# Kernel tuning notes

Hardware: AMD Instinct MI355X
Metric: run time of the kernel (lower is better)

The kernel has to match this reference:

```python
import jax, jax.numpy as jnp
import numpy as np

LAYERS, BLOCKS = 10, 4
RC, DC, SC, EC = 32, 32, 256, 256  # residual, dilation, skip, end channels
CIN, COUT, K = 6, 1, 2
DILATIONS = [2 ** (i % LAYERS) for i in range(BLOCKS * LAYERS)]
NL = len(DILATIONS)


def conv1d(x, w, dilation=1, pad=0):
    # x: [N, C, T], w: [O, I, K]
    return jax.lax.conv_general_dilated(
        x, w, window_strides=(1,), padding=[(pad, pad)],
        rhs_dilation=(dilation,), dimension_numbers=('NCH', 'OIH', 'NCH'))


def setup_inputs() -> dict:
    key = jax.random.key(0)
    ks = jax.random.split(key, 10)
    s = 0.1
    return {
        'x': jax.random.normal(ks[0], (8, CIN, 8192), dtype=jnp.float32),
        'start_w': jax.random.normal(ks[1], (RC, CIN, 1), dtype=jnp.float32) * s,
        'filter_w': jax.random.normal(ks[2], (NL, DC, RC, K), dtype=jnp.float32) * s,
        'gate_w': jax.random.normal(ks[3], (NL, DC, RC, K), dtype=jnp.float32) * s,
        'res_w': jax.random.normal(ks[4], (NL, RC, DC, 1), dtype=jnp.float32) * s,
        'skip_w': jax.random.normal(ks[5], (NL, SC, DC, 1), dtype=jnp.float32) * s,
        'end1_w': jax.random.normal(ks[6], (EC, SC, 1), dtype=jnp.float32) * s,
        'end1_b': jax.random.normal(ks[7], (EC,), dtype=jnp.float32) * s,
        'end2_w': jax.random.normal(ks[8], (COUT, EC, 1), dtype=jnp.float32) * s,
        'end2_b': jax.random.normal(ks[9], (COUT,), dtype=jnp.float32) * s,
    }


def reference(x, start_w, filter_w, gate_w, res_w, skip_w, end1_w, end1_b, end2_w, end2_b):
    x = conv1d(x, start_w)  # [B, RC, T]
    T = x.shape[2]
    # symmetric padding=(K-1)*d makes length grow by d each layer;
    # the shortest skip is the first one: T + (K-1)*DILATIONS[0]
    min_len = T + (K - 1) * DILATIONS[0]
    skip_sum = jnp.zeros((x.shape[0], SC, min_len), dtype=x.dtype)
    for i, d in enumerate(DILATIONS):
        pad = (K - 1) * d
        f = jnp.tanh(conv1d(x, filter_w[i], d, pad))
        g = jax.nn.sigmoid(conv1d(x, gate_w[i], d, pad))
        x = f * g  # [B, DC, T'] with T' = T_prev + d
        s = conv1d(x, skip_w[i])
        skip_sum = skip_sum + s[:, :, -min_len:]
        x = conv1d(x, res_w[i]) + x  # residual add (RC == DC)
    h = jax.nn.relu(skip_sum)
    h = jax.nn.relu(conv1d(h, end1_w) + end1_b[None, :, None])
    h = conv1d(h, end2_w) + end2_b[None, :, None]
    return h[:, :, -1]  # [B, COUT]
```

## Files before the change

kernel.cpp:

```cpp
#include <hip/hip_runtime.h>
#include <hip/hip_fp16.h>
#include <math.h>


#define NL 40
#define TLEN 8192

#define F_BLOB 0
#define F_C0   40960
#define F_Z    41216
#define F_H    51456
#define F_OB   53504
#define F_CNT  53512
#define F_DUMP 60000

typedef __attribute__((ext_vector_type(2))) _Float16 h2;

#if defined(__has_builtin)
#if __has_builtin(__builtin_amdgcn_fdot2)
#define HAS_FDOT2 1
#endif
#endif

__device__ __forceinline__ float FDOT2(h2 a, h2 b, float c) {
#ifdef HAS_FDOT2
    return __builtin_amdgcn_fdot2(a, b, c, false);
#else
    return c + (float)a.x * (float)b.x + (float)a.y * (float)b.y;
#endif
}

__device__ __forceinline__ float tanh_fast(float f) {
    f = fminf(fmaxf(f, -15.f), 15.f);
    float e2 = __expf(2.f * f);
    return (e2 - 1.f) / (e2 + 1.f);
}

__global__ __launch_bounds__(256) void k1_fold(
    const float* __restrict__ x, const float* __restrict__ start_w,
    const float* __restrict__ filter_w, const float* __restrict__ gate_w,
    const float* __restrict__ res_w, float* __restrict__ ws)
{
    const int l = blockIdx.x, m = blockIdx.y;
    const int t = threadIdx.x;

    if (l == NL) {
        if (m == 0) {
            const int b = t >> 5, ch = t & 31;
            float acc = 0.f;
#pragma unroll
            for (int j = 0; j < 6; ++j)
                acc += start_w[ch * 6 + j] * x[(b * 6 + j) * TLEN + TLEN - 1];
            ws[F_C0 + t] = acc;
            if (t < 8) { ws[F_OB + t] = 0.f; ((int*)(ws + F_CNT))[t] = 0; }
        } else {
            for (int k = t; k < 2048; k += 256) ws[F_H + k] = 0.f;
        }
        return;
    }

    __shared__ float F[32][32];
    __shared__ __align__(16) float R[32][36];
    const float* src = m ? gate_w : filter_w;
    for (int e = t; e < 1024; e += 256)
        F[e >> 5][e & 31] = src[(l * 1024 + e) * 2];
    if (l > 0)
        for (int e = t; e < 1024; e += 256) {
            const int k = e >> 5, j = e & 31;
            R[k][j] = res_w[(l - 1) * 1024 + e] + (k == j ? 1.f : 0.f);
        }
    __syncthreads();

    const int ch = t >> 3, jg = t & 7, j0 = jg * 4;
    float o0, o1, o2, o3;
    if (l == 0) {
        o0 = F[ch][j0]; o1 = F[ch][j0+1]; o2 = F[ch][j0+2]; o3 = F[ch][j0+3];
    } else {
        o0 = o1 = o2 = o3 = 0.f;
#pragma unroll
        for (int k = 0; k < 32; ++k) {
            const float fv = F[ch][k];
            const float4 rv = *(const float4*)&R[k][j0];
            o0 += fv * rv.x; o1 += fv * rv.y; o2 += fv * rv.z; o3 += fv * rv.w;
        }
    }
    const int hh = jg >> 2;
    __half* dst = (__half*)ws + (size_t)l * 2048 + (hh * 32 + ch) * 32
                + (m ? 16 : 0) + (j0 & 15);
    ((__half2*)dst)[0] = __floats2half2_rn(o0, o1);
    ((__half2*)dst)[1] = __floats2half2_rn(o2, o3);
}

#define K2_PREF(L, W) do {                                                   \
    if ((L) < NL) {                                                          \
        _Pragma("unroll")                                                    \
        for (int i = 0; i < 4; ++i)                                          \
            W[i] = blob[(L) * 256 + lane * 4 + i];                           \
    }                                                                        \
} while (0)

#define K2_STEP(L, W) do {                                                   \
         \
    float zx = __shfl_xor(z, 1, 64);                                         \
    float ze = (ch & 1) ? zx : z;                                            \
    float zo = (ch & 1) ? z  : zx;                                           \
    __half2 pk = __halves2half2(__float2half(ze), __float2half(zo));         \
    int pki; __builtin_memcpy(&pki, &pk, 4);                                 \
    h2 sv[8];                                                                \
    _Pragma("unroll")                                                        \
    for (int i = 0; i < 8; ++i) {                                            \
        int q = __shfl(pki, hbase + 2 * i, 64);                              \
        __builtin_memcpy(&sv[i], &q, 4);                                     \
    }                                                                        \
    float f = 0.f, g = 0.f;                                                  \
    const h2* wf = (const h2*)&W[0];                                         \
    const h2* wg = (const h2*)&W[2];                                         \
    _Pragma("unroll")                                                        \
    for (int i = 0; i < 8; ++i) {                                            \
        f = FDOT2(wf[i], sv[i], f);                                          \
        g = FDOT2(wg[i], sv[i], g);                                          \
    }                                                                        \
    f += __shfl_xor(f, 32, 64);                                              \
    g += __shfl_xor(g, 32, 64);                                              \
    z = tanh_fast(f) * (1.f / (1.f + __expf(-g)));                           \
    if (h == 0) zbuf[((L) * 8 + b) * 32 + ch] = z;                           \
    K2_PREF((L) + 4, W);                                                     \
} while (0)

__global__ __launch_bounds__(256) void k2_recur(
    const float* __restrict__ skip_w, const float* __restrict__ end1_w,
    const float* __restrict__ end1_b, const float* __restrict__ end2_w,
    float* __restrict__ ws)
{
    const int bi = blockIdx.x, t = threadIdx.x;

    if (bi >= 8) {
        const int wi = (bi - 8) * 256 + t;
        const float4* s4 = (const float4*)skip_w;
        const float4* e4 = (const float4*)end1_w;
        float acc = 0.f;
        for (int i = wi; i < 81920; i += 32768) acc += s4[i].x;
        if (wi < 16384) acc += e4[wi].x;
        if (wi < 64) acc += end2_w[wi * 4] + end1_b[wi * 4];
        if (acc == 1234.567f) ws[F_DUMP] = acc;
        return;
    }
    if (t >= 64) return;

    const int b = bi, lane = t;
    const int ch = lane & 31, h = lane >> 5, hbase = h << 4;
    float* zbuf = ws + F_Z;
    float z = ws[F_C0 + b * 32 + ch];

    const float4* blob = (const float4*)ws;
    float4 w0[4], w1[4], w2[4], w3[4];
    K2_PREF(0, w0); K2_PREF(1, w1); K2_PREF(2, w2); K2_PREF(3, w3);
    for (int l = 0; l < NL; l += 4) {
        K2_STEP(l + 0, w0);
        K2_STEP(l + 1, w1);
        K2_STEP(l + 2, w2);
        K2_STEP(l + 3, w3);
    }
}

__global__ __launch_bounds__(256) void k3a_skip(
    const float* __restrict__ skip_w, float* __restrict__ ws)
{
    const int l = blockIdx.x, b = blockIdx.y, t = threadIdx.x;
    __shared__ __align__(16) float zsm[32];
    if (t < 32) zsm[t] = ws[F_Z + (l * 8 + b) * 32 + t];
    __syncthreads();
    const float4* w4 = (const float4*)(skip_w + (size_t)(l * 256 + t) * 32);
    const float4* z4 = (const float4*)zsm;
    float acc = 0.f;
#pragma unroll
    for (int i = 0; i < 8; ++i) {
        float4 wv = w4[i], zv = z4[i];
        acc += wv.x*zv.x + wv.y*zv.y + wv.z*zv.z + wv.w*zv.w;
    }
    atomicAdd(&ws[F_H + b * 256 + t], acc);
}

__global__ __launch_bounds__(256) void k3b_end(
    const float* __restrict__ end1_w, const float* __restrict__ end1_b,
    const float* __restrict__ end2_w, const float* __restrict__ end2_b,
    float* __restrict__ ws, float* __restrict__ out)
{
    const int q = blockIdx.x, b = blockIdx.y, t = threadIdx.x;
    __shared__ __align__(16) float hsm[256];
    __shared__ float psum[64][5];
    const int p = t >> 6, oc = t & 63, row = q * 64 + oc;

    float4 wreg[16];
    const float4* wp = (const float4*)(end1_w + (size_t)row * 256 + p * 64);
#pragma unroll
    for (int i = 0; i < 16; ++i) wreg[i] = wp[i];

    hsm[t] = fmaxf(ws[F_H + b * 256 + t], 0.f);
    __syncthreads();
    const float4* h4 = (const float4*)(hsm + p * 64);
    float acc = 0.f;
#pragma unroll
    for (int i = 0; i < 16; ++i) {
        float4 wv = wreg[i], hv = h4[i];
        acc += wv.x*hv.x + wv.y*hv.y + wv.z*hv.z + wv.w*hv.w;
    }
    psum[oc][p] = acc;
    __syncthreads();
    if (t < 64) {
        const int rr = q * 64 + t;
        float e = psum[t][0] + psum[t][1] + psum[t][2] + psum[t][3]
                + end1_b[rr];
        e = fmaxf(e, 0.f);
        float pe = e * end2_w[rr];
#pragma unroll
        for (int off = 32; off > 0; off >>= 1)
            pe += __shfl_down(pe, off, 64);
        if (t == 0) {
            float* obuf = ws + F_OB;
            int* cnt = (int*)(ws + F_CNT);
            atomicAdd(&obuf[b], pe);
            __threadfence();
            int old = __hip_atomic_fetch_add(&cnt[b], 1, __ATOMIC_ACQ_REL,
                                             __HIP_MEMORY_SCOPE_AGENT);
            if (old == 3) {
                float tot = __hip_atomic_load(&obuf[b], __ATOMIC_ACQUIRE,
                                              __HIP_MEMORY_SCOPE_AGENT);
                out[b] = tot + end2_b[0];
            }
        }
    }
}

extern "C" void kernel_launch(void* const* d_in, const int* in_sizes, int n_in,
                              void* d_out, int out_size, void* d_ws, size_t ws_size,
                              hipStream_t stream) {
    const float* x        = (const float*)d_in[0];
    const float* start_w  = (const float*)d_in[1];
    const float* filter_w = (const float*)d_in[2];
    const float* gate_w   = (const float*)d_in[3];
    const float* res_w    = (const float*)d_in[4];
    const float* skip_w   = (const float*)d_in[5];
    const float* end1_w   = (const float*)d_in[6];
    const float* end1_b   = (const float*)d_in[7];
    const float* end2_w   = (const float*)d_in[8];
    const float* end2_b   = (const float*)d_in[9];
    float* out = (float*)d_out;
    float* ws  = (float*)d_ws;

    k1_fold <<<dim3(NL + 1, 2), 256, 0, stream>>>(x, start_w, filter_w,
                                                  gate_w, res_w, ws);
    k2_recur<<<136, 256, 0, stream>>>(skip_w, end1_w, end1_b, end2_w, ws);
    k3a_skip<<<dim3(NL, 8), 256, 0, stream>>>(skip_w, ws);
    k3b_end <<<dim3(4, 8), 256, 0, stream>>>(end1_w, end1_b, end2_w, end2_b,
                                             ws, out);
}
```

Baseline: 98.44 us.

## Fuse skip accumulation and end MLP into one kernel with last-block election

```diff
diff --git a/kernel.cpp b/kernel.cpp
--- a/kernel.cpp
+++ b/kernel.cpp
@@ -135,14 +135,16 @@
     const int bi = blockIdx.x, t = threadIdx.x;
 
     if (bi >= 8) {
-        const int wi = (bi - 8) * 256 + t;
+        const int g  = bi & 7;
+        const int wg = (bi - 8) >> 3;
+        const int li = wg * 256 + t;
         const float4* s4 = (const float4*)skip_w;
         const float4* e4 = (const float4*)end1_w;
         float acc = 0.f;
-        for (int i = wi; i < 81920; i += 32768) acc += s4[i].x;
-        if (wi < 16384) acc += e4[wi].x;
-        if (wi < 64) acc += end2_w[wi * 4] + end1_b[wi * 4];
-        if (acc == 1234.567f) ws[F_DUMP] = acc;
+        for (int i = li; i < 81920; i += 4096) acc += s4[i].x;
+        for (int i = li; i < 16384; i += 4096) acc += e4[i].x;
+        if (li < 64) acc += end2_w[li * 4] + end1_b[li * 4];
+        if (acc == 1234.567f) ws[F_DUMP + g] = acc;
         return;
     }
     if (t >= 64) return;
@@ -163,73 +165,64 @@
     }
 }
 
-__global__ __launch_bounds__(256) void k3a_skip(
-    const float* __restrict__ skip_w, float* __restrict__ ws)
-{
-    const int l = blockIdx.x, b = blockIdx.y, t = threadIdx.x;
-    __shared__ __align__(16) float zsm[32];
-    if (t < 32) zsm[t] = ws[F_Z + (l * 8 + b) * 32 + t];
-    __syncthreads();
-    const float4* w4 = (const float4*)(skip_w + (size_t)(l * 256 + t) * 32);
-    const float4* z4 = (const float4*)zsm;
-    float acc = 0.f;
-#pragma unroll
-    for (int i = 0; i < 8; ++i) {
-        float4 wv = w4[i], zv = z4[i];
-        acc += wv.x*zv.x + wv.y*zv.y + wv.z*zv.z + wv.w*zv.w;
-    }
-    atomicAdd(&ws[F_H + b * 256 + t], acc);
-}
-
-__global__ __launch_bounds__(256) void k3b_end(
+__global__ __launch_bounds__(256) void k3_skipend(
+    const float* __restrict__ skip_w,
     const float* __restrict__ end1_w, const float* __restrict__ end1_b,
     const float* __restrict__ end2_w, const float* __restrict__ end2_b,
     float* __restrict__ ws, float* __restrict__ out)
 {
-    const int q = blockIdx.x, b = blockIdx.y, t = threadIdx.x;
+    const int l = blockIdx.x, b = blockIdx.y, t = threadIdx.x;
+    __shared__ __align__(16) float zsm[32];
     __shared__ __align__(16) float hsm[256];
-    __shared__ float psum[64][5];
-    const int p = t >> 6, oc = t & 63, row = q * 64 + oc;
-
-    float4 wreg[16];
-    const float4* wp = (const float4*)(end1_w + (size_t)row * 256 + p * 64);
-#pragma unroll
-    for (int i = 0; i < 16; ++i) wreg[i] = wp[i];
-
-    hsm[t] = fmaxf(ws[F_H + b * 256 + t], 0.f);
-    __syncthreads();
-    const float4* h4 = (const float4*)(hsm + p * 64);
-    float acc = 0.f;
-#pragma unroll
-    for (int i = 0; i < 16; ++i) {
-        float4 wv = wreg[i], hv = h4[i];
-        acc += wv.x*hv.x + wv.y*hv.y + wv.z*hv.z + wv.w*hv.w;
-    }
-    psum[oc][p] = acc;
-    __syncthreads();
-    if (t < 64) {
-        const int rr = q * 64 + t;
-        float e = psum[t][0] + psum[t][1] + psum[t][2] + psum[t][3]
-                + end1_b[rr];
-        e = fmaxf(e, 0.f);
-        float pe = e * end2_w[rr];
-#pragma unroll
-        for (int off = 32; off > 0; off >>= 1)
-            pe += __shfl_down(pe, off, 64);
-        if (t == 0) {
-            float* obuf = ws + F_OB;
-            int* cnt = (int*)(ws + F_CNT);
-            atomicAdd(&obuf[b], pe);
-            __threadfence();
-            int old = __hip_atomic_fetch_add(&cnt[b], 1, __ATOMIC_ACQ_REL,
-                                             __HIP_MEMORY_SCOPE_AGENT);
-            if (old == 3) {
-                float tot = __hip_atomic_load(&obuf[b], __ATOMIC_ACQUIRE,
-                                              __HIP_MEMORY_SCOPE_AGENT);
-                out[b] = tot + end2_b[0];
-            }
-        }
-    }
+    __shared__ float psum[4];
+    __shared__ int elect;
+
+    if (t < 32) zsm[t] = ws[F_Z + (l * 8 + b) * 32 + t];
+    __syncthreads();
+    {
+        const float4* w4 = (const float4*)(skip_w + (size_t)(l * 256 + t) * 32);
+        const float4* z4 = (const float4*)zsm;
+        float acc = 0.f;
+#pragma unroll
+        for (int i = 0; i < 8; ++i) {
+            float4 wv = w4[i], zv = z4[i];
+            acc += wv.x*zv.x + wv.y*zv.y + wv.z*zv.z + wv.w*zv.w;
+        }
+        atomicAdd(&ws[F_H + b * 256 + t], acc);
+    }
+    __syncthreads();
+    if (t == 0) {
+        __threadfence();
+        int* cnt = (int*)(ws + F_CNT);
+        int old = __hip_atomic_fetch_add(&cnt[b], 1, __ATOMIC_ACQ_REL,
+                                         __HIP_MEMORY_SCOPE_AGENT);
+        elect = (old == NL - 1);
+    }
+    __syncthreads();
+    if (!elect) return;
+
+    float hv = __hip_atomic_load((const float*)&ws[F_H + b * 256 + t],
+                                 __ATOMIC_ACQUIRE, __HIP_MEMORY_SCOPE_AGENT);
+    hsm[t] = fmaxf(hv, 0.f);
+    __syncthreads();
+
+    float e = 0.f;
+    const float4* w1p = (const float4*)(end1_w + (size_t)t * 256);
+    const float4* h4 = (const float4*)hsm;
+#pragma unroll
+    for (int i = 0; i < 64; ++i) {
+        float4 wv = w1p[i], hv4 = h4[i];
+        e += wv.x*hv4.x + wv.y*hv4.y + wv.z*hv4.z + wv.w*hv4.w;
+    }
+    e = fmaxf(e + end1_b[t], 0.f);
+    float pe = e * end2_w[t];
+#pragma unroll
+    for (int off = 32; off > 0; off >>= 1)
+        pe += __shfl_down(pe, off, 64);
+    if ((t & 63) == 0) psum[t >> 6] = pe;
+    __syncthreads();
+    if (t == 0)
+        out[b] = psum[0] + psum[1] + psum[2] + psum[3] + end2_b[0];
 }
 
 extern "C" void kernel_launch(void* const* d_in, const int* in_sizes, int n_in,
@@ -248,10 +241,9 @@
     float* out = (float*)d_out;
     float* ws  = (float*)d_ws;
 
-    k1_fold <<<dim3(NL + 1, 2), 256, 0, stream>>>(x, start_w, filter_w,
-                                                  gate_w, res_w, ws);
-    k2_recur<<<136, 256, 0, stream>>>(skip_w, end1_w, end1_b, end2_w, ws);
-    k3a_skip<<<dim3(NL, 8), 256, 0, stream>>>(skip_w, ws);
-    k3b_end <<<dim3(4, 8), 256, 0, stream>>>(end1_w, end1_b, end2_w, end2_b,
-                                             ws, out);
-}
+    k1_fold   <<<dim3(NL + 1, 2), 256, 0, stream>>>(x, start_w, filter_w,
+                                                    gate_w, res_w, ws);
+    k2_recur  <<<136, 256, 0, stream>>>(skip_w, end1_w, end1_b, end2_w, ws);
+    k3_skipend<<<dim3(NL, 8), 256, 0, stream>>>(skip_w, end1_w, end1_b,
+                                                end2_w, end2_b, ws, out);
+}
```

Measured after the change: 109.6 us. +11.3%, slower.
